# Kernel optimization log

Hardware: AMD Instinct MI355X
Metric: run time of the kernel (lower is better)

## Reference

```python
import jax, jax.numpy as jnp
import numpy as np

EPS = 1e-05
RFN = 0.5  # blend factor between group-norm path and per-token layer-norm path


def _ln_last(x, eps):
    # layer_norm over last dim, no affine (matches F.layer_norm(x, x.shape[-1:]))
    mu = jnp.mean(x, axis=-1, keepdims=True)
    var = jnp.mean(jnp.square(x - mu), axis=-1, keepdims=True)
    return (x - mu) * jax.lax.rsqrt(var + eps)


def setup_inputs() -> dict:
    key = jax.random.key(0)
    kx, kw, kb = jax.random.split(key, 3)
    B, T, D, G = 8, 4000, 1024, 5
    x = jax.random.normal(kx, (B, T, D), dtype=jnp.float32)
    mask = jnp.ones((G, T // G), dtype=jnp.int32)  # default dense mask: 5 contiguous groups
    weight = jax.random.normal(kw, (D,), dtype=jnp.float32)
    bias = jax.random.normal(kb, (D,), dtype=jnp.float32)
    return {"x": x, "mask": mask, "weight": weight, "bias": bias}


def reference(x, mask, weight, bias):
    B, T, D = x.shape
    G = mask.shape[0]          # number of groups from mask rows
    L = T // G                 # tokens per group (dense ones mask => contiguous blocks)

    # rfn_mode == 'in': per-token layer norm over feature dim
    lned = _ln_last(x, EPS)

    # per-group layer norm over (group_tokens, features) jointly, matching
    # F.layer_norm(x[:, i], normalized_shape=x[:, i].shape[-2:])
    xg = x.reshape(B, G, L, D)
    mu = jnp.mean(xg, axis=(-2, -1), keepdims=True)
    var = jnp.mean(jnp.square(xg - mu), axis=(-2, -1), keepdims=True)
    gn = ((xg - mu) * jax.lax.rsqrt(var + EPS)).reshape(B, T, D)

    return (RFN * gn + (1.0 - RFN) * lned) * weight + bias
```

## Files before the change

kernel.cpp:

```cpp
#include <hip/hip_runtime.h>


#define EPS 1e-5f
#define NUM_G 5

__global__ __launch_bounds__(256) void stats_kernel(
    const float4* __restrict__ x, float2* __restrict__ tstats) {
  const int wave = threadIdx.x >> 6, lane = threadIdx.x & 63;
  const int row = blockIdx.x * 4 + wave;
  const long base = (long)row * 256;

  float s = 0.f, sq = 0.f;
  #pragma unroll
  for (int j = 0; j < 4; ++j) {
    float4 v = x[base + lane + 64 * j];
    s  += (v.x + v.y) + (v.z + v.w);
    sq += (v.x * v.x + v.y * v.y) + (v.z * v.z + v.w * v.w);
  }
  #pragma unroll
  for (int off = 1; off < 64; off <<= 1) {
    s  += __shfl_xor(s,  off, 64);
    sq += __shfl_xor(sq, off, 64);
  }
  if (lane == 0) {
    float2 st; st.x = s; st.y = sq;
    tstats[row] = st;
  }
}

__global__ __launch_bounds__(256) void greduce_kernel(
    const float2* __restrict__ tstats, float2* __restrict__ gstats,
    int L, float invNg) {
  const int g = blockIdx.x;
  float s = 0.f, sq = 0.f;
  for (int j = threadIdx.x; j < L; j += 256) {
    float2 st = tstats[(long)g * L + j];
    s += st.x; sq += st.y;
  }
  #pragma unroll
  for (int off = 1; off < 64; off <<= 1) {
    s  += __shfl_xor(s,  off, 64);
    sq += __shfl_xor(sq, off, 64);
  }
  __shared__ float ls[4], lq[4];
  const int wave = threadIdx.x >> 6, lane = threadIdx.x & 63;
  if (lane == 0) { ls[wave] = s; lq[wave] = sq; }
  __syncthreads();
  if (threadIdx.x == 0) {
    const float S  = (ls[0] + ls[1]) + (ls[2] + ls[3]);
    const float SQ = (lq[0] + lq[1]) + (lq[2] + lq[3]);
    const float gmu = S * invNg;
    float2 o;
    o.x = gmu;
    o.y = rsqrtf(SQ * invNg - gmu * gmu + EPS) * 0.5f;
    gstats[g] = o;
  }
}

__global__ __launch_bounds__(256) void out_kernel(
    const float4* __restrict__ x, const float2* __restrict__ gstats,
    const float2* __restrict__ tstats,
    const float4* __restrict__ weight, const float4* __restrict__ bias,
    float4* __restrict__ out, int L, float invD) {
  const int tid = threadIdx.x;
  const float4 w  = weight[tid];
  const float4 bb = bias[tid];
  const int row0 = blockIdx.x * 4;

  #pragma unroll
  for (int r = 0; r < 4; ++r) {
    const int row = row0 + r;
    const float2 gst = gstats[row / L];
    const float gmu = gst.x, grs = gst.y;
    const float2 st = tstats[row];
    const float tmu = st.x * invD;
    const float trs = rsqrtf(st.y * invD - tmu * tmu + EPS) * 0.5f;

    const long base = (long)row * 256;
    const float4 v = x[base + tid];
    float4 o;
    o.x = ((v.x - gmu) * grs + (v.x - tmu) * trs) * w.x + bb.x;
    o.y = ((v.y - gmu) * grs + (v.y - tmu) * trs) * w.y + bb.y;
    o.z = ((v.z - gmu) * grs + (v.z - tmu) * trs) * w.z + bb.z;
    o.w = ((v.w - gmu) * grs + (v.w - tmu) * trs) * w.w + bb.w;
    out[base + tid] = o;
  }
}

extern "C" void kernel_launch(void* const* d_in, const int* in_sizes, int n_in,
                              void* d_out, int out_size, void* d_ws, size_t ws_size,
                              hipStream_t stream) {
  const float* x      = (const float*)d_in[0];
  const float* weight = (const float*)d_in[2];
  const float* bias   = (const float*)d_in[3];
  float* out          = (float*)d_out;

  const int D = in_sizes[2];
  const int T = in_sizes[1];
  const int B = in_sizes[0] / (T * D);
  const int L = T / NUM_G;
  const int n_rows = B * T;
  const long Ng = (long)L * D;

  float2* tstats = (float2*)d_ws;
  float2* gstats = (float2*)((char*)d_ws + (size_t)n_rows * sizeof(float2));

  dim3 blk(256);
  stats_kernel<<<dim3(n_rows / 4), blk, 0, stream>>>((const float4*)x, tstats);

  greduce_kernel<<<dim3(B * NUM_G), blk, 0, stream>>>(
      tstats, gstats, L, 1.0f / (float)Ng);

  out_kernel<<<dim3(n_rows / 4), blk, 0, stream>>>(
      (const float4*)x, gstats, tstats,
      (const float4*)weight, (const float4*)bias,
      (float4*)out, L, 1.0f / D);
}
```

Measured before the change: 246.8 us.

## Fuse three normalization kernels into one cooperative persistent kernel with grid syncs

Replaces the stats, group-reduce and output kernels with a single cooperative kernel of 1024 persistent blocks. Two grid-wide barriers separate the per-row stats pass, the per-group reduction and the normalize-and-write pass. This removes two kernel launch boundaries and their gaps. In exchange it adds grid barrier overhead, leaves most blocks idle during the group reduction, and fixes the grid size. The second read of x (131 MB) likely still misses cache, so the pass stays memory-bound.

```diff
diff --git a/kernel.cpp b/kernel.cpp
--- a/kernel.cpp
+++ b/kernel.cpp
@@ -1,118 +1,124 @@
 #include <hip/hip_runtime.h>
+#include <hip/hip_cooperative_groups.h>
+
+namespace cg = cooperative_groups;
 
 
 #define EPS 1e-5f
 #define NUM_G 5
+#define NBLK 1024
+#define NTHR 256
 
-__global__ __launch_bounds__(256) void stats_kernel(
-    const float4* __restrict__ x, float2* __restrict__ tstats) {
-  const int wave = threadIdx.x >> 6, lane = threadIdx.x & 63;
-  const int row = blockIdx.x * 4 + wave;
-  const long base = (long)row * 256;
+__global__ __launch_bounds__(NTHR, 4) void rfnorm_fused(
+    const float4* __restrict__ x,
+    const float4* __restrict__ weight, const float4* __restrict__ bias,
+    float4* __restrict__ out,
+    float2* __restrict__ tstats, float2* __restrict__ gstats,
+    int n_rows, int L, float invD, float invNg) {
+  const int tid  = threadIdx.x;
+  const int wave = tid >> 6, lane = tid & 63;
 
-  float s = 0.f, sq = 0.f;
-  #pragma unroll
-  for (int j = 0; j < 4; ++j) {
-    float4 v = x[base + lane + 64 * j];
-    s  += (v.x + v.y) + (v.z + v.w);
-    sq += (v.x * v.x + v.y * v.y) + (v.z * v.z + v.w * v.w);
+  const int n_waves = gridDim.x * (NTHR / 64);
+  for (int row = blockIdx.x * (NTHR / 64) + wave; row < n_rows; row += n_waves) {
+    const long base = (long)row * 256;
+    float s = 0.f, sq = 0.f;
+    #pragma unroll
+    for (int j = 0; j < 4; ++j) {
+      float4 v = x[base + lane + 64 * j];
+      s  += (v.x + v.y) + (v.z + v.w);
+      sq += (v.x * v.x + v.y * v.y) + (v.z * v.z + v.w * v.w);
+    }
+    #pragma unroll
+    for (int off = 1; off < 64; off <<= 1) {
+      s  += __shfl_xor(s,  off, 64);
+      sq += __shfl_xor(sq, off, 64);
+    }
+    if (lane == 0) { float2 st; st.x = s; st.y = sq; tstats[row] = st; }
   }
-  #pragma unroll
-  for (int off = 1; off < 64; off <<= 1) {
-    s  += __shfl_xor(s,  off, 64);
-    sq += __shfl_xor(sq, off, 64);
+
+  __threadfence();
+  cg::this_grid().sync();
+
+  const int n_groups = n_rows / L;
+  if ((int)blockIdx.x < n_groups) {
+    const int g = blockIdx.x;
+    float s = 0.f, sq = 0.f;
+    for (int j = tid; j < L; j += NTHR) {
+      float2 st = tstats[(long)g * L + j];
+      s += st.x; sq += st.y;
+    }
+    #pragma unroll
+    for (int off = 1; off < 64; off <<= 1) {
+      s  += __shfl_xor(s,  off, 64);
+      sq += __shfl_xor(sq, off, 64);
+    }
+    __shared__ float ls[4], lq[4];
+    if (lane == 0) { ls[wave] = s; lq[wave] = sq; }
+    __syncthreads();
+    if (tid == 0) {
+      const float S  = (ls[0] + ls[1]) + (ls[2] + ls[3]);
+      const float SQ = (lq[0] + lq[1]) + (lq[2] + lq[3]);
+      const float gmu = S * invNg;
+      float2 o;
+      o.x = gmu;
+      o.y = rsqrtf(SQ * invNg - gmu * gmu + EPS) * 0.5f;
+      gstats[g] = o;
+    }
   }
-  if (lane == 0) {
-    float2 st; st.x = s; st.y = sq;
-    tstats[row] = st;
-  }
-}
 
-__global__ __launch_bounds__(256) void greduce_kernel(
-    const float2* __restrict__ tstats, float2* __restrict__ gstats,
-    int L, float invNg) {
-  const int g = blockIdx.x;
-  float s = 0.f, sq = 0.f;
-  for (int j = threadIdx.x; j < L; j += 256) {
-    float2 st = tstats[(long)g * L + j];
-    s += st.x; sq += st.y;
-  }
-  #pragma unroll
-  for (int off = 1; off < 64; off <<= 1) {
-    s  += __shfl_xor(s,  off, 64);
-    sq += __shfl_xor(sq, off, 64);
-  }
-  __shared__ float ls[4], lq[4];
-  const int wave = threadIdx.x >> 6, lane = threadIdx.x & 63;
-  if (lane == 0) { ls[wave] = s; lq[wave] = sq; }
-  __syncthreads();
-  if (threadIdx.x == 0) {
-    const float S  = (ls[0] + ls[1]) + (ls[2] + ls[3]);
-    const float SQ = (lq[0] + lq[1]) + (lq[2] + lq[3]);
-    const float gmu = S * invNg;
-    float2 o;
-    o.x = gmu;
-    o.y = rsqrtf(SQ * invNg - gmu * gmu + EPS) * 0.5f;
-    gstats[g] = o;
-  }
-}
+  __threadfence();
+  cg::this_grid().sync();
 
-__global__ __launch_bounds__(256) void out_kernel(
-    const float4* __restrict__ x, const float2* __restrict__ gstats,
-    const float2* __restrict__ tstats,
-    const float4* __restrict__ weight, const float4* __restrict__ bias,
-    float4* __restrict__ out, int L, float invD) {
-  const int tid = threadIdx.x;
   const float4 w  = weight[tid];
   const float4 bb = bias[tid];
-  const int row0 = blockIdx.x * 4;
+  const int n_chunks = n_rows >> 2;
+  for (int c = blockIdx.x; c < n_chunks; c += gridDim.x) {
+    const int row0 = c << 2;
+    #pragma unroll
+    for (int r = 0; r < 4; ++r) {
+      const int row = row0 + r;
+      const float2 gst = gstats[row / L];
+      const float gmu = gst.x, grs = gst.y;
+      const float2 st = tstats[row];
+      const float tmu = st.x * invD;
+      const float trs = rsqrtf(st.y * invD - tmu * tmu + EPS) * 0.5f;
 
-  #pragma unroll
-  for (int r = 0; r < 4; ++r) {
-    const int row = row0 + r;
-    const float2 gst = gstats[row / L];
-    const float gmu = gst.x, grs = gst.y;
-    const float2 st = tstats[row];
-    const float tmu = st.x * invD;
-    const float trs = rsqrtf(st.y * invD - tmu * tmu + EPS) * 0.5f;
-
-    const long base = (long)row * 256;
-    const float4 v = x[base + tid];
-    float4 o;
-    o.x = ((v.x - gmu) * grs + (v.x - tmu) * trs) * w.x + bb.x;
-    o.y = ((v.y - gmu) * grs + (v.y - tmu) * trs) * w.y + bb.y;
-    o.z = ((v.z - gmu) * grs + (v.z - tmu) * trs) * w.z + bb.z;
-    o.w = ((v.w - gmu) * grs + (v.w - tmu) * trs) * w.w + bb.w;
-    out[base + tid] = o;
+      const long base = (long)row * 256;
+      const float4 v = x[base + tid];
+      float4 o;
+      o.x = ((v.x - gmu) * grs + (v.x - tmu) * trs) * w.x + bb.x;
+      o.y = ((v.y - gmu) * grs + (v.y - tmu) * trs) * w.y + bb.y;
+      o.z = ((v.z - gmu) * grs + (v.z - tmu) * trs) * w.z + bb.z;
+      o.w = ((v.w - gmu) * grs + (v.w - tmu) * trs) * w.w + bb.w;
+      out[base + tid] = o;
+    }
   }
 }
 
 extern "C" void kernel_launch(void* const* d_in, const int* in_sizes, int n_in,
                               void* d_out, int out_size, void* d_ws, size_t ws_size,
                               hipStream_t stream) {
-  const float* x      = (const float*)d_in[0];
-  const float* weight = (const float*)d_in[2];
-  const float* bias   = (const float*)d_in[3];
-  float* out          = (float*)d_out;
+  const float4* x      = (const float4*)d_in[0];
+  const float4* weight = (const float4*)d_in[2];
+  const float4* bias   = (const float4*)d_in[3];
+  float4* out          = (float4*)d_out;
 
   const int D = in_sizes[2];
   const int T = in_sizes[1];
   const int B = in_sizes[0] / (T * D);
-  const int L = T / NUM_G;
-  const int n_rows = B * T;
+  int L      = T / NUM_G;
+  int n_rows = B * T;
   const long Ng = (long)L * D;
 
   float2* tstats = (float2*)d_ws;
   float2* gstats = (float2*)((char*)d_ws + (size_t)n_rows * sizeof(float2));
 
-  dim3 blk(256);
-  stats_kernel<<<dim3(n_rows / 4), blk, 0, stream>>>((const float4*)x, tstats);
+  float invD  = 1.0f / (float)D;
+  float invNg = 1.0f / (float)Ng;
 
-  greduce_kernel<<<dim3(B * NUM_G), blk, 0, stream>>>(
-      tstats, gstats, L, 1.0f / (float)Ng);
-
-  out_kernel<<<dim3(n_rows / 4), blk, 0, stream>>>(
-      (const float4*)x, gstats, tstats,
-      (const float4*)weight, (const float4*)bias,
-      (float4*)out, L, 1.0f / D);
+  void* args[] = {(void*)&x, (void*)&weight, (void*)&bias, (void*)&out,
+                  (void*)&tstats, (void*)&gstats,
+                  (void*)&n_rows, (void*)&L, (void*)&invD, (void*)&invNg};
+  hipLaunchCooperativeKernel((const void*)rfnorm_fused, dim3(NBLK), dim3(NTHR),
+                             args, 0, stream);
 }
```

Result: slower. 603.2 us (+144.4%).
